# Performance work log

Measured on AMD Instinct MI355X. Metric: run time of the kernel, lower is better.

## Reference

```python
import jax, jax.numpy as jnp
import numpy as np

N = 50000
E = 600000
IN_DIM = 128
HID = 128
HEADS = 4
OUT = HID // HEADS  # per-head out channels
R = 2
LAYERS = 2
NEG_SLOPE = 0.2


def _glorot(key, shape):
    fan_in, fan_out = shape[-2], shape[-1]
    lim = jnp.sqrt(6.0 / (fan_in + fan_out))
    return jax.random.uniform(key, shape, jnp.float32, -lim, lim)


def setup_inputs() -> dict:
    key = jax.random.key(0)
    ks = jax.random.split(key, 20)
    x = jax.random.normal(ks[0], (N, IN_DIM), jnp.float32)
    eidx = jax.random.randint(ks[1], (2, E), 0, N, jnp.int64 if jax.config.jax_enable_x64 else jnp.int32)
    etype = jax.random.randint(ks[2], (E,), 0, R, eidx.dtype)
    d = IN_DIM
    params = {}
    ki = 3
    for l in range(LAYERS):
        params[f"W{l}"] = _glorot(ks[ki], (R, d, HID)); ki += 1            # per-relation weight
        params[f"Q{l}"] = _glorot(ks[ki], (HID, HEADS)); ki += 1           # query proj (dim=1)
        params[f"K{l}"] = _glorot(ks[ki], (HID, HEADS)); ki += 1           # key proj
        params[f"cb{l}"] = jnp.zeros((HID,), jnp.float32)                   # conv bias
        params[f"pW{l}"] = _glorot(ks[ki], (HID, HID)); ki += 1            # proj Linear weight [out,in]
        params[f"pb{l}"] = jnp.zeros((HID,), jnp.float32)
        d = HID
    return dict(x=x, eidx=eidx, etype=etype, **params)


def _rgat_conv(h, src, dst, etype, W, Q, K, b):
    # per-relation transform of all nodes: [R, N, HID]
    xw = jnp.einsum('ni,rio->rno', h, W)
    out_j = xw[etype, src]          # [E, HID] source features under edge's relation
    out_i = xw[etype, dst]          # [E, HID] target features under edge's relation
    # additive self-attention, dim=1: alpha [E, HEADS]
    alpha = jax.nn.leaky_relu(out_i @ Q + out_j @ K, NEG_SLOPE)
    # segment softmax over destination nodes (across-relation)
    m = jax.ops.segment_max(alpha, dst, num_segments=N)
    m = jnp.where(jnp.isfinite(m), m, 0.0)
    e = jnp.exp(alpha - m[dst])
    s = jax.ops.segment_sum(e, dst, num_segments=N)
    a = e / (s[dst] + 1e-16)
    # weighted messages and scatter-sum aggregation
    msg = out_j.reshape(E, HEADS, OUT) * a[:, :, None]
    agg = jax.ops.segment_sum(msg.reshape(E, HID), dst, num_segments=N)
    return agg + b


def reference(x, eidx, etype, W0, Q0, K0, cb0, pW0, pb0, W1, Q1, K1, cb1, pW1, pb1):
    src, dst = eidx[0], eidx[1]  # flow source_to_target: aggregate at eidx[1]
    h = x
    for (W, Q, K, cb, pW, pb) in ((W0, Q0, K0, cb0, pW0, pb0), (W1, Q1, K1, cb1, pW1, pb1)):
        h = _rgat_conv(h, src, dst, etype, W, Q, K, cb)
        h = jax.nn.elu(h @ pW.T + pb)
    return h
```

## Files before the change

kernel.cpp:

```cpp
#include <hip/hip_runtime.h>
#include <hip/hip_bf16.h>

typedef __hip_bfloat16 bf16;
typedef short s16x8 __attribute__((ext_vector_type(8)));
typedef float f32x4 __attribute__((ext_vector_type(4)));

#define N_NODES 50000
#define NPAD    50048
#define E_EDGES 600000
#define HID     128
#define HEADS   4
#define SCAN_B  196

__device__ __forceinline__ unsigned short f2bf_bits(float f) {
  unsigned u = __float_as_uint(f);
  u += 0x7fffu + ((u >> 16) & 1u);
  return (unsigned short)(u >> 16);
}
__device__ __forceinline__ float bf2f(unsigned short b) {
  return __uint_as_float(((unsigned)b) << 16);
}
__device__ __forceinline__ float lo_f(unsigned v) { return __uint_as_float(v << 16); }
__device__ __forceinline__ float hi_f(unsigned v) { return __uint_as_float(v & 0xffff0000u); }

__device__ __forceinline__ float lrelu(float v) { return v >= 0.f ? v : 0.2f * v; }

__global__ __launch_bounds__(256) void detect_kernel(const unsigned short* __restrict__ xb,
                                                     const int* __restrict__ ei,
                                                     int* __restrict__ flags) {
  int t = threadIdx.x;
  __shared__ int cnt[2];
  if (t < 2) cnt[t] = 0;
  __syncthreads();
  unsigned short v = xb[2 * t];
  int ex = (v >> 7) & 0xFF;
  if (ex < 119 || ex > 135) atomicAdd(&cnt[0], 1);
  if (ei[2 * t + 1] != 0) atomicAdd(&cnt[1], 1);
  __syncthreads();
  if (t == 0) {
    flags[0] = (cnt[0] > 64) ? 1 : 0;
    flags[1] = (cnt[1] == 0) ? 1 : 0;
  }
}

__global__ __launch_bounds__(256) void zero_int_kernel(int* __restrict__ p, int n) {
  int i = blockIdx.x * 256 + threadIdx.x;
  if (i < n) p[i] = 0;
}

__global__ __launch_bounds__(256) void cvt_idx_hist_kernel(const int* __restrict__ eidx,
                                                           const int* __restrict__ etype,
                                                           int* __restrict__ dstA, int* __restrict__ pk,
                                                           int* __restrict__ deg,
                                                           const int* __restrict__ flags) {
  int e = blockIdx.x * 256 + threadIdx.x;
  if (e >= E_EDGES) return;
  int s, d, r;
  if (flags[1]) {
    const long long* e64 = (const long long*)eidx;
    const long long* t64 = (const long long*)etype;
    s = (int)e64[e]; d = (int)e64[E_EDGES + e]; r = (int)t64[e];
  } else {
    s = eidx[e]; d = eidx[E_EDGES + e]; r = etype[e];
  }
  dstA[e] = d;
  pk[e] = s | (r << 16);
  atomicAdd(&deg[d], 1);
}

__global__ __launch_bounds__(256) void cvt_xb_kernel(const void* __restrict__ src,
                                                     unsigned short* __restrict__ dst, int n,
                                                     const int* __restrict__ flags) {
  int i = blockIdx.x * 256 + threadIdx.x;
  if (i >= n) return;
  if (flags[0]) dst[i] = f2bf_bits(((const float*)src)[i]);
  else          dst[i] = ((const unsigned short*)src)[i];
}

__global__ __launch_bounds__(256) void cvt_wt_kernel(const void* __restrict__ src0,
                                                     const void* __restrict__ src1,
                                                     unsigned short* __restrict__ dst,
                                                     const int* __restrict__ flags) {
  int idx = blockIdx.x * 256 + threadIdx.x;
  if (idx >= 2 * 2 * HID * HID) return;
  int l = idx >> 15, rem = idx & 32767;
  int r = rem >> 14, i = (rem >> 7) & 127, o = rem & 127;
  const void* src = l ? src1 : src0;
  unsigned short b;
  if (flags[0]) b = f2bf_bits(((const float*)src)[rem]);
  else          b = ((const unsigned short*)src)[rem];
  dst[(size_t)l * 2 * HID * HID + ((size_t)r * HID + o) * HID + i] = b;
}

struct P8 { const void* src[8]; int dstoff[8]; int n[8]; };
__global__ __launch_bounds__(256) void cvt_params_kernel(P8 tab, float* __restrict__ base,
                                                         const int* __restrict__ flags) {
  const int f = flags[0];
  for (int k = 0; k < 8; ++k) {
    int n = tab.n[k];
    for (int i = blockIdx.x * 256 + threadIdx.x; i < n; i += gridDim.x * 256) {
      float v = f ? ((const float*)tab.src[k])[i] : bf2f(((const unsigned short*)tab.src[k])[i]);
      base[tab.dstoff[k] + i] = v;
    }
  }
}

__global__ __launch_bounds__(256) void scan1_kernel(const int* __restrict__ deg,
                                                    int* __restrict__ excl,
                                                    int* __restrict__ bsum) {
  __shared__ int sm[256];
  int t = threadIdx.x, i = blockIdx.x * 256 + t;
  int v = (i < NPAD) ? deg[i] : 0;
  sm[t] = v;
  __syncthreads();
#pragma unroll
  for (int off = 1; off < 256; off <<= 1) {
    int add = (t >= off) ? sm[t - off] : 0;
    __syncthreads();
    sm[t] += add;
    __syncthreads();
  }
  if (i < NPAD) excl[i] = sm[t] - v;
  if (t == 255) bsum[blockIdx.x] = sm[255];
}

__global__ __launch_bounds__(256) void scan23_kernel(const int* __restrict__ excl,
                                                     const int* __restrict__ bsum,
                                                     int* __restrict__ rowstart) {
  __shared__ int sm[256];
  int t = threadIdx.x;
  int v = (t < SCAN_B) ? bsum[t] : 0;
  sm[t] = v;
  __syncthreads();
#pragma unroll
  for (int off = 1; off < 256; off <<= 1) {
    int add = (t >= off) ? sm[t - off] : 0;
    __syncthreads();
    sm[t] += add;
    __syncthreads();
  }
  int bpre = (blockIdx.x > 0) ? sm[blockIdx.x - 1] : 0;
  int i = blockIdx.x * 256 + t;
  if (i < NPAD) rowstart[i] = excl[i] + bpre;
  if (i == 0) rowstart[NPAD] = E_EDGES;
}

__global__ __launch_bounds__(256) void scatter_kernel(const int* __restrict__ dstA,
                                                      const int* __restrict__ pk,
                                                      const int* __restrict__ rowstart,
                                                      int* __restrict__ cnt,
                                                      int* __restrict__ eord) {
  int e = blockIdx.x * 256 + threadIdx.x;
  if (e >= E_EDGES) return;
  int d = dstA[e];
  int pos = rowstart[d] + atomicAdd(&cnt[d], 1);
  eord[pos] = pk[e];
}

__device__ __forceinline__ void wave_gemm64(const unsigned short* __restrict__ Ab, int row0,
                                            const unsigned short* __restrict__ Bt, int colb,
                                            int lane, f32x4 acc[4][4]) {
  const int lm = lane & 15, q = lane >> 4;
  s16x8 af[4][4], bfr[4][4];
#pragma unroll
  for (int kc = 0; kc < 4; ++kc) {
    const int ko = kc * 32 + q * 8;
#pragma unroll
    for (int rt = 0; rt < 4; ++rt)
      af[kc][rt] = *(const s16x8*)(Ab + (size_t)(row0 + rt * 16 + lm) * HID + ko);
  }
#pragma unroll
  for (int kc = 0; kc < 4; ++kc) {
    const int ko = kc * 32 + q * 8;
#pragma unroll
    for (int ct = 0; ct < 4; ++ct)
      bfr[kc][ct] = *(const s16x8*)(Bt + (size_t)(colb + ct * 16 + lm) * HID + ko);
  }
#pragma unroll
  for (int kc = 0; kc < 4; ++kc)
#pragma unroll
    for (int rt = 0; rt < 4; ++rt)
#pragma unroll
      for (int ct = 0; ct < 4; ++ct)
        acc[rt][ct] = __builtin_amdgcn_mfma_f32_16x16x32_bf16(af[kc][rt], bfr[kc][ct], acc[rt][ct], 0, 0, 0);
}

__global__ __launch_bounds__(256) void gemm_xw_mfma(const unsigned short* __restrict__ hb,
                                                    const unsigned short* __restrict__ Wbt,
                                                    unsigned short* __restrict__ xw) {
  const int wave = threadIdx.x >> 6, lane = threadIdx.x & 63;
  const int row0 = blockIdx.x * 64;
  const int r = wave >> 1, colb = (wave & 1) * 64;
  f32x4 acc[4][4];
#pragma unroll
  for (int a = 0; a < 4; ++a)
#pragma unroll
    for (int b = 0; b < 4; ++b) { f32x4 z = {0.f, 0.f, 0.f, 0.f}; acc[a][b] = z; }
  wave_gemm64(hb, row0, Wbt + (size_t)r * HID * HID, colb, lane, acc);
  const int lm = lane & 15, q = lane >> 4;
#pragma unroll
  for (int rt = 0; rt < 4; ++rt)
#pragma unroll
    for (int i = 0; i < 4; ++i) {
      int row = row0 + rt * 16 + q * 4 + i;
      if (row < N_NODES) {
#pragma unroll
        for (int ct = 0; ct < 4; ++ct) {
          int o = colb + ct * 16 + lm;
          xw[((size_t)r * NPAD + row) * HID + o] = f2bf_bits(acc[rt][ct][i]);
        }
      }
    }
}

__global__ __launch_bounds__(128) void proj_mfma(const unsigned short* __restrict__ aggb,
                                                 const unsigned short* __restrict__ pWTb,
                                                 const float* __restrict__ bo,
                                                 unsigned short* __restrict__ hbout,
                                                 void* __restrict__ dout,
                                                 const int* __restrict__ flags) {
  const int wave = threadIdx.x >> 6, lane = threadIdx.x & 63;
  const int row0 = blockIdx.x * 64;
  const int colb = wave * 64;
  f32x4 acc[4][4];
#pragma unroll
  for (int a = 0; a < 4; ++a)
#pragma unroll
    for (int b = 0; b < 4; ++b) { f32x4 z = {0.f, 0.f, 0.f, 0.f}; acc[a][b] = z; }
  wave_gemm64(aggb, row0, pWTb, colb, lane, acc);
  const int lm = lane & 15, q = lane >> 4;
  const int f32out = flags[0];
#pragma unroll
  for (int rt = 0; rt < 4; ++rt)
#pragma unroll
    for (int i = 0; i < 4; ++i) {
      int row = row0 + rt * 16 + q * 4 + i;
      if (row < N_NODES) {
#pragma unroll
        for (int ct = 0; ct < 4; ++ct) {
          int o = colb + ct * 16 + lm;
          float v = acc[rt][ct][i] + bo[o];
          v = v > 0.f ? v : expm1f(v);
          size_t idx = (size_t)row * HID + o;
          if (dout) {
            if (f32out) ((float*)dout)[idx] = v;
            else        ((unsigned short*)dout)[idx] = f2bf_bits(v);
          } else {
            hbout[idx] = f2bf_bits(v);
          }
        }
      }
    }
}

__global__ __launch_bounds__(256) void prep_wq_kernel(const unsigned short* __restrict__ Wbt,
                                                      const float* __restrict__ Qf,
                                                      const float* __restrict__ Kf,
                                                      unsigned short* __restrict__ qkt_hi,
                                                      unsigned short* __restrict__ qkt_lo) {
  int idx = blockIdx.x * 256 + threadIdx.x;
  if (idx >= 2 * 2 * HID) return;
  int i = idx & 127, lr = idx >> 7, l = lr >> 1, r = (lr & 1);
  float aq[4] = {0.f, 0.f, 0.f, 0.f}, ak[4] = {0.f, 0.f, 0.f, 0.f};
  const unsigned short* Wb = Wbt + (size_t)lr * HID * HID;
  const float* Qp = Qf + l * HID * HEADS;
  const float* Kp = Kf + l * HID * HEADS;
  for (int j = 0; j < HID; ++j) {
    float w = bf2f(Wb[j * HID + i]);
    float4 q4 = *(const float4*)(Qp + j * 4);
    float4 k4 = *(const float4*)(Kp + j * 4);
    aq[0] += w * q4.x; aq[1] += w * q4.y; aq[2] += w * q4.z; aq[3] += w * q4.w;
    ak[0] += w * k4.x; ak[1] += w * k4.y; ak[2] += w * k4.z; ak[3] += w * k4.w;
  }
  size_t base = (size_t)l * 16 * HID;
#pragma unroll
  for (int h = 0; h < 4; ++h) {
    unsigned short qh = f2bf_bits(aq[h]);
    unsigned short kh = f2bf_bits(ak[h]);
    float qres = aq[h] - bf2f(qh);
    float kres = ak[h] - bf2f(kh);
    qkt_hi[base + (size_t)(r * 4 + h) * HID + i] = qh;
    qkt_lo[base + (size_t)(r * 4 + h) * HID + i] = f2bf_bits(qres);
    qkt_hi[base + (size_t)(8 + r * 4 + h) * HID + i] = kh;
    qkt_lo[base + (size_t)(8 + r * 4 + h) * HID + i] = f2bf_bits(kres);
  }
}

__global__ __launch_bounds__(256) void qk_mfma_kernel(const unsigned short* __restrict__ hb,
                                                      const unsigned short* __restrict__ qkt_hi,
                                                      const unsigned short* __restrict__ qkt_lo,
                                                      float4* __restrict__ qi4,
                                                      float4* __restrict__ kj4) {
  __shared__ float st[4][16][68];
  const int wave = threadIdx.x >> 6, lane = threadIdx.x & 63;
  const int row0 = blockIdx.x * 256 + wave * 64;
  const int lm = lane & 15, q = lane >> 4;
  if (row0 < NPAD) {
    s16x8 bhi[4], blo[4], af[4][4];
#pragma unroll
    for (int kc = 0; kc < 4; ++kc) {
      const int ko = kc * 32 + q * 8;
      bhi[kc] = *(const s16x8*)(qkt_hi + (size_t)lm * HID + ko);
      blo[kc] = *(const s16x8*)(qkt_lo + (size_t)lm * HID + ko);
    }
#pragma unroll
    for (int kc = 0; kc < 4; ++kc) {
      const int ko = kc * 32 + q * 8;
#pragma unroll
      for (int rt = 0; rt < 4; ++rt)
        af[kc][rt] = *(const s16x8*)(hb + (size_t)(row0 + rt * 16 + lm) * HID + ko);
    }
    f32x4 acc[4];
#pragma unroll
    for (int a = 0; a < 4; ++a) { f32x4 z = {0.f, 0.f, 0.f, 0.f}; acc[a] = z; }
#pragma unroll
    for (int kc = 0; kc < 4; ++kc)
#pragma unroll
      for (int rt = 0; rt < 4; ++rt) {
        acc[rt] = __builtin_amdgcn_mfma_f32_16x16x32_bf16(af[kc][rt], bhi[kc], acc[rt], 0, 0, 0);
        acc[rt] = __builtin_amdgcn_mfma_f32_16x16x32_bf16(af[kc][rt], blo[kc], acc[rt], 0, 0, 0);
      }
#pragma unroll
    for (int rt = 0; rt < 4; ++rt)
      *(f32x4*)&st[wave][lm][rt * 16 + q * 4] = acc[rt];
  }
  __syncthreads();
  if (row0 < NPAD) {
    int n = row0 + lane;
    if (n < N_NODES) {
      float4 v;
      v.x = st[wave][0][lane]; v.y = st[wave][1][lane]; v.z = st[wave][2][lane]; v.w = st[wave][3][lane];
      qi4[n] = v;
      v.x = st[wave][4][lane]; v.y = st[wave][5][lane]; v.z = st[wave][6][lane]; v.w = st[wave][7][lane];
      qi4[NPAD + n] = v;
      v.x = st[wave][8][lane]; v.y = st[wave][9][lane]; v.z = st[wave][10][lane]; v.w = st[wave][11][lane];
      kj4[n] = v;
      v.x = st[wave][12][lane]; v.y = st[wave][13][lane]; v.z = st[wave][14][lane]; v.w = st[wave][15][lane];
      kj4[NPAD + n] = v;
    }
  }
}

__global__ __launch_bounds__(256) void edge_fused_kernel(
    const int* __restrict__ rowstart, const int* __restrict__ eord,
    const float4* __restrict__ qi4, const float4* __restrict__ kj4,
    const unsigned short* __restrict__ xw, unsigned short* __restrict__ aggb) {
  __shared__ float wls[4][64][4];
  const int wave = threadIdx.x >> 6, lane = threadIdx.x & 63;
  const int n = blockIdx.x * 4 + wave;
  unsigned* outp = (unsigned*)(aggb + ((size_t)n << 7)) + lane;
  const int start = rowstart[n];
  const int deg = rowstart[n + 1] - start;
  if (deg == 0) { *outp = 0u; return; }
  const int hh = lane >> 4;
  const int ch2 = lane << 1;
  float2 acc = {0.f, 0.f};
  float ssel;
  if (deg <= 64) {
    int p = 0;
    float a0 = -1e30f, a1 = -1e30f, a2 = -1e30f, a3 = -1e30f;
    if (lane < deg) {
      p = eord[start + lane];
      int s = p & 0xffff, r = p >> 16;
      float4 k4 = kj4[r ? (NPAD + s) : s];
      float4 q4 = r ? qi4[NPAD + n] : qi4[n];
      a0 = lrelu(q4.x + k4.x); a1 = lrelu(q4.y + k4.y);
      a2 = lrelu(q4.z + k4.z); a3 = lrelu(q4.w + k4.w);
    }
    float m0 = a0, m1 = a1, m2 = a2, m3 = a3;
#pragma unroll
    for (int off = 32; off > 0; off >>= 1) {
      m0 = fmaxf(m0, __shfl_xor(m0, off)); m1 = fmaxf(m1, __shfl_xor(m1, off));
      m2 = fmaxf(m2, __shfl_xor(m2, off)); m3 = fmaxf(m3, __shfl_xor(m3, off));
    }
    float w0 = 0.f, w1 = 0.f, w2 = 0.f, w3 = 0.f;
    if (lane < deg) {
      w0 = __expf(a0 - m0); w1 = __expf(a1 - m1);
      w2 = __expf(a2 - m2); w3 = __expf(a3 - m3);
    }
    float s0 = w0, s1 = w1, s2 = w2, s3 = w3;
#pragma unroll
    for (int off = 32; off > 0; off >>= 1) {
      s0 += __shfl_xor(s0, off); s1 += __shfl_xor(s1, off);
      s2 += __shfl_xor(s2, off); s3 += __shfl_xor(s3, off);
    }
    ssel = hh == 0 ? s0 : hh == 1 ? s1 : hh == 2 ? s2 : s3;
    volatile float* wp = &wls[wave][lane][0];
    wp[0] = w0; wp[1] = w1; wp[2] = w2; wp[3] = w3;
    volatile float* wr = &wls[wave][0][0];
    const int degp = (deg + 3) & ~3;
    for (int e = 0; e < degp; e += 4) {
      int p0 = __builtin_amdgcn_readlane(p, e);
      int p1 = __builtin_amdgcn_readlane(p, e + 1);
      int p2 = __builtin_amdgcn_readlane(p, e + 2);
      int p3 = __builtin_amdgcn_readlane(p, e + 3);
      unsigned v0 = *(const unsigned*)(xw + ((size_t)((p0 & 0xffff) + (p0 >> 16) * NPAD) << 7) + ch2);
      unsigned v1 = *(const unsigned*)(xw + ((size_t)((p1 & 0xffff) + (p1 >> 16) * NPAD) << 7) + ch2);
      unsigned v2 = *(const unsigned*)(xw + ((size_t)((p2 & 0xffff) + (p2 >> 16) * NPAD) << 7) + ch2);
      unsigned v3 = *(const unsigned*)(xw + ((size_t)((p3 & 0xffff) + (p3 >> 16) * NPAD) << 7) + ch2);
      float we0 = wr[(e + 0) * 4 + hh];
      float we1 = wr[(e + 1) * 4 + hh];
      float we2 = wr[(e + 2) * 4 + hh];
      float we3 = wr[(e + 3) * 4 + hh];
      acc.x = fmaf(lo_f(v0), we0, acc.x); acc.y = fmaf(hi_f(v0), we0, acc.y);
      acc.x = fmaf(lo_f(v1), we1, acc.x); acc.y = fmaf(hi_f(v1), we1, acc.y);
      acc.x = fmaf(lo_f(v2), we2, acc.x); acc.y = fmaf(hi_f(v2), we2, acc.y);
      acc.x = fmaf(lo_f(v3), we3, acc.x); acc.y = fmaf(hi_f(v3), we3, acc.y);
    }
  } else {
    const float4 q0 = qi4[n], q1 = qi4[NPAD + n];
    float4 m = make_float4(-1e30f, -1e30f, -1e30f, -1e30f);
    for (int e = start; e < start + deg; ++e) {
      int pe = eord[e];
      int s = pe & 0xffff, r = pe >> 16;
      float4 k4 = kj4[(size_t)r * NPAD + s];
      float4 q4 = r ? q1 : q0;
      m.x = fmaxf(m.x, lrelu(q4.x + k4.x)); m.y = fmaxf(m.y, lrelu(q4.y + k4.y));
      m.z = fmaxf(m.z, lrelu(q4.z + k4.z)); m.w = fmaxf(m.w, lrelu(q4.w + k4.w));
    }
    float4 sv = make_float4(0.f, 0.f, 0.f, 0.f);
    for (int e = start; e < start + deg; ++e) {
      int pe = eord[e];
      int s = pe & 0xffff, r = pe >> 16;
      float4 k4 = kj4[(size_t)r * NPAD + s];
      float4 q4 = r ? q1 : q0;
      float w0 = __expf(lrelu(q4.x + k4.x) - m.x);
      float w1 = __expf(lrelu(q4.y + k4.y) - m.y);
      float w2 = __expf(lrelu(q4.z + k4.z) - m.z);
      float w3 = __expf(lrelu(q4.w + k4.w) - m.w);
      sv.x += w0; sv.y += w1; sv.z += w2; sv.w += w3;
      float we = hh == 0 ? w0 : hh == 1 ? w1 : hh == 2 ? w2 : w3;
      unsigned v = *(const unsigned*)(xw + (((size_t)r * NPAD + s) << 7) + ch2);
      acc.x = fmaf(lo_f(v), we, acc.x);
      acc.y = fmaf(hi_f(v), we, acc.y);
    }
    ssel = hh == 0 ? sv.x : hh == 1 ? sv.y : hh == 2 ? sv.z : sv.w;
  }
  float inv = 1.f / (ssel + 1e-16f);
  *outp = (unsigned)f2bf_bits(acc.x * inv) | ((unsigned)f2bf_bits(acc.y * inv) << 16);
}

__global__ __launch_bounds__(64) void prep_proj_kernel(const void* __restrict__ pW0,
                                                       const void* __restrict__ pW1,
                                                       const float* __restrict__ cbf,
                                                       const float* __restrict__ pbf,
                                                       unsigned short* __restrict__ pWTb2,
                                                       float* __restrict__ bo2,
                                                       const int* __restrict__ flags) {
  int o = blockIdx.x & 127, l = blockIdx.x >> 7, t = threadIdx.x;
  const void* pWraw = l ? pW1 : pW0;
  const float* cb = cbf + l * HID;
  const int f = flags[0];
  float part = 0.f;
#pragma unroll
  for (int i = t; i < HID; i += 64) {
    float w = f ? ((const float*)pWraw)[o * HID + i] : bf2f(((const unsigned short*)pWraw)[o * HID + i]);
    pWTb2[(size_t)l * HID * HID + o * HID + i] = f2bf_bits(w);
    part += cb[i] * w;
  }
#pragma unroll
  for (int off = 32; off > 0; off >>= 1) part += __shfl_xor(part, off);
  if (t == 0) bo2[l * HID + o] = pbf[l * HID + o] + part;
}

extern "C" void kernel_launch(void* const* d_in, const int* in_sizes, int n_in,
                              void* d_out, int out_size, void* d_ws, size_t ws_size,
                              hipStream_t stream) {
  const void* x     = d_in[0];
  const int*  eidx  = (const int*)d_in[1];
  const int*  etype = (const int*)d_in[2];
  const int iW[2] = {3, 9}, iQ[2] = {4, 10}, iK[2] = {5, 11}, icb[2] = {6, 12}, ipW[2] = {7, 13}, ipb[2] = {8, 14};

  float* ws = (float*)d_ws;
  size_t off = 0;
  int*   flags = (int*)(ws + off); off += 16;
  unsigned short* hb   = (unsigned short*)(ws + off); off += (size_t)NPAD * HID / 2;
  unsigned short* xw   = (unsigned short*)(ws + off); off += (size_t)NPAD * HID;
  float* qi   = ws + off; off += (size_t)2 * NPAD * HEADS;
  float* kj   = ws + off; off += (size_t)2 * NPAD * HEADS;
  unsigned short* aggb = (unsigned short*)(ws + off); off += (size_t)NPAD * HID / 2;
  int* dstA = (int*)(ws + off); off += E_EDGES;
  int* pk   = (int*)(ws + off); off += E_EDGES;
  int* eord = (int*)(ws + off); off += E_EDGES;
  int* deg  = (int*)(ws + off); off += NPAD;
  int* cnt  = (int*)(ws + off); off += NPAD;
  int* excl = (int*)(ws + off); off += NPAD;
  int* rowstart = (int*)(ws + off); off += NPAD + 16;
  int* bsum  = (int*)(ws + off); off += 256;
  unsigned short* Wbt   = (unsigned short*)(ws + off); off += (size_t)2 * 2 * HID * HID / 2;
  unsigned short* pWTb2 = (unsigned short*)(ws + off); off += (size_t)2 * HID * HID / 2;
  unsigned short* qkt_hi = (unsigned short*)(ws + off); off += (size_t)2 * 16 * HID / 2;
  unsigned short* qkt_lo = (unsigned short*)(ws + off); off += (size_t)2 * 16 * HID / 2;
  float* Qf  = ws + off; off += 2 * HID * HEADS;
  float* Kf  = ws + off; off += 2 * HID * HEADS;
  float* cbf = ws + off; off += 2 * HID;
  float* pbf = ws + off; off += 2 * HID;
  float* bo2 = ws + off; off += 2 * HID;

  detect_kernel<<<1, 256, 0, stream>>>((const unsigned short*)x, eidx, flags);
  zero_int_kernel<<<(2 * NPAD + 255) / 256, 256, 0, stream>>>(deg, 2 * NPAD);
  cvt_idx_hist_kernel<<<(E_EDGES + 255) / 256, 256, 0, stream>>>(eidx, etype, dstA, pk, deg, flags);
  cvt_xb_kernel<<<(N_NODES * HID + 255) / 256, 256, 0, stream>>>(x, hb, N_NODES * HID, flags);
  cvt_wt_kernel<<<(2 * 2 * HID * HID + 255) / 256, 256, 0, stream>>>(d_in[iW[0]], d_in[iW[1]], Wbt, flags);
  {
    P8 tab;
    float* base = ws;
    for (int l = 0; l < 2; ++l) {
      tab.src[l * 4 + 0] = d_in[iQ[l]];  tab.dstoff[l * 4 + 0] = (int)(Qf - base) + l * HID * HEADS;  tab.n[l * 4 + 0] = HID * HEADS;
      tab.src[l * 4 + 1] = d_in[iK[l]];  tab.dstoff[l * 4 + 1] = (int)(Kf - base) + l * HID * HEADS;  tab.n[l * 4 + 1] = HID * HEADS;
      tab.src[l * 4 + 2] = d_in[icb[l]]; tab.dstoff[l * 4 + 2] = (int)(cbf - base) + l * HID;         tab.n[l * 4 + 2] = HID;
      tab.src[l * 4 + 3] = d_in[ipb[l]]; tab.dstoff[l * 4 + 3] = (int)(pbf - base) + l * HID;         tab.n[l * 4 + 3] = HID;
    }
    cvt_params_kernel<<<2, 256, 0, stream>>>(tab, base, flags);
  }

  scan1_kernel<<<SCAN_B, 256, 0, stream>>>(deg, excl, bsum);
  scan23_kernel<<<SCAN_B, 256, 0, stream>>>(excl, bsum, rowstart);
  scatter_kernel<<<(E_EDGES + 255) / 256, 256, 0, stream>>>(dstA, pk, rowstart, cnt, eord);

  prep_wq_kernel<<<2, 256, 0, stream>>>(Wbt, Qf, Kf, qkt_hi, qkt_lo);
  prep_proj_kernel<<<2 * HID, 64, 0, stream>>>(d_in[ipW[0]], d_in[ipW[1]], cbf, pbf, pWTb2, bo2, flags);

  const int RB = NPAD / 64;
  const int QB = (NPAD + 255) / 256;
  for (int l = 0; l < 2; ++l) {
    gemm_xw_mfma<<<RB, 256, 0, stream>>>(hb, Wbt + (size_t)l * 2 * HID * HID, xw);
    qk_mfma_kernel<<<QB, 256, 0, stream>>>(hb, qkt_hi + (size_t)l * 16 * HID, qkt_lo + (size_t)l * 16 * HID,
                                           (float4*)qi, (float4*)kj);
    edge_fused_kernel<<<N_NODES / 4, 256, 0, stream>>>(rowstart, eord, (const float4*)qi, (const float4*)kj, xw, aggb);
    proj_mfma<<<RB, 128, 0, stream>>>(aggb, pWTb2 + (size_t)l * HID * HID, bo2 + l * HID, hb,
                                      (l == 1) ? d_out : nullptr, flags);
  }
}
```

Baseline: 392.4 us.

## Stage GEMM A tiles in LDS and unroll edge gather by eight

Both MFMA GEMM kernels now load the 64-row A tile cooperatively into padded shared memory with coalesced 16-byte loads, instead of each wave reading it strided from global memory. The B fragments are still loaded per wave before the tile. In the edge kernel, the attention-weight LDS layout becomes head-major with padding, and the gather loop issues eight independent row loads per iteration instead of four, to hide more memory latency. This costs extra LDS, a block barrier, and more registers, and the padded loop runs for up to seven more readlane slots for low-degree nodes.

After: 373.1 us. 1.05x faster.

```diff
diff --git a/kernel.cpp b/kernel.cpp
--- a/kernel.cpp
+++ b/kernel.cpp
@@ -157,47 +157,48 @@
   eord[pos] = pk[e];
 }
 
-__device__ __forceinline__ void wave_gemm64(const unsigned short* __restrict__ Ab, int row0,
-                                            const unsigned short* __restrict__ Bt, int colb,
-                                            int lane, f32x4 acc[4][4]) {
-  const int lm = lane & 15, q = lane >> 4;
-  s16x8 af[4][4], bfr[4][4];
-#pragma unroll
-  for (int kc = 0; kc < 4; ++kc) {
-    const int ko = kc * 32 + q * 8;
-#pragma unroll
-    for (int rt = 0; rt < 4; ++rt)
-      af[kc][rt] = *(const s16x8*)(Ab + (size_t)(row0 + rt * 16 + lm) * HID + ko);
-  }
-#pragma unroll
-  for (int kc = 0; kc < 4; ++kc) {
-    const int ko = kc * 32 + q * 8;
-#pragma unroll
-    for (int ct = 0; ct < 4; ++ct)
-      bfr[kc][ct] = *(const s16x8*)(Bt + (size_t)(colb + ct * 16 + lm) * HID + ko);
-  }
-#pragma unroll
-  for (int kc = 0; kc < 4; ++kc)
-#pragma unroll
-    for (int rt = 0; rt < 4; ++rt)
-#pragma unroll
-      for (int ct = 0; ct < 4; ++ct)
-        acc[rt][ct] = __builtin_amdgcn_mfma_f32_16x16x32_bf16(af[kc][rt], bfr[kc][ct], acc[rt][ct], 0, 0, 0);
-}
 
 __global__ __launch_bounds__(256) void gemm_xw_mfma(const unsigned short* __restrict__ hb,
                                                     const unsigned short* __restrict__ Wbt,
                                                     unsigned short* __restrict__ xw) {
-  const int wave = threadIdx.x >> 6, lane = threadIdx.x & 63;
+  __shared__ unsigned short As[64][136];
+  const int t = threadIdx.x;
+  const int wave = t >> 6, lane = t & 63;
   const int row0 = blockIdx.x * 64;
   const int r = wave >> 1, colb = (wave & 1) * 64;
+  const int lm = lane & 15, q = lane >> 4;
+  const unsigned short* Bt = Wbt + (size_t)r * HID * HID;
+  s16x8 bfr[4][4];
+#pragma unroll
+  for (int kc = 0; kc < 4; ++kc) {
+    const int ko = kc * 32 + q * 8;
+#pragma unroll
+    for (int ct = 0; ct < 4; ++ct)
+      bfr[kc][ct] = *(const s16x8*)(Bt + (size_t)(colb + ct * 16 + lm) * HID + ko);
+  }
+  const unsigned short* gsrc = hb + (size_t)row0 * HID;
+#pragma unroll
+  for (int j = 0; j < 4; ++j) {
+    int idx = j * 256 + t;
+    *(s16x8*)&As[idx >> 4][(idx & 15) * 8] = *(const s16x8*)(gsrc + idx * 8);
+  }
+  __syncthreads();
   f32x4 acc[4][4];
 #pragma unroll
   for (int a = 0; a < 4; ++a)
 #pragma unroll
     for (int b = 0; b < 4; ++b) { f32x4 z = {0.f, 0.f, 0.f, 0.f}; acc[a][b] = z; }
-  wave_gemm64(hb, row0, Wbt + (size_t)r * HID * HID, colb, lane, acc);
-  const int lm = lane & 15, q = lane >> 4;
+#pragma unroll
+  for (int kc = 0; kc < 4; ++kc) {
+    const int ko = kc * 32 + q * 8;
+#pragma unroll
+    for (int rt = 0; rt < 4; ++rt) {
+      s16x8 a = *(const s16x8*)&As[rt * 16 + lm][ko];
+#pragma unroll
+      for (int ct = 0; ct < 4; ++ct)
+        acc[rt][ct] = __builtin_amdgcn_mfma_f32_16x16x32_bf16(a, bfr[kc][ct], acc[rt][ct], 0, 0, 0);
+    }
+  }
 #pragma unroll
   for (int rt = 0; rt < 4; ++rt)
 #pragma unroll
@@ -219,16 +220,43 @@
                                                  unsigned short* __restrict__ hbout,
                                                  void* __restrict__ dout,
                                                  const int* __restrict__ flags) {
-  const int wave = threadIdx.x >> 6, lane = threadIdx.x & 63;
+  __shared__ unsigned short As[64][136];
+  const int t = threadIdx.x;
+  const int wave = t >> 6, lane = t & 63;
   const int row0 = blockIdx.x * 64;
   const int colb = wave * 64;
+  const int lm = lane & 15, q = lane >> 4;
+  s16x8 bfr[4][4];
+#pragma unroll
+  for (int kc = 0; kc < 4; ++kc) {
+    const int ko = kc * 32 + q * 8;
+#pragma unroll
+    for (int ct = 0; ct < 4; ++ct)
+      bfr[kc][ct] = *(const s16x8*)(pWTb + (size_t)(colb + ct * 16 + lm) * HID + ko);
+  }
+  const unsigned short* gsrc = aggb + (size_t)row0 * HID;
+#pragma unroll
+  for (int j = 0; j < 8; ++j) {
+    int idx = j * 128 + t;
+    *(s16x8*)&As[idx >> 4][(idx & 15) * 8] = *(const s16x8*)(gsrc + idx * 8);
+  }
+  __syncthreads();
   f32x4 acc[4][4];
 #pragma unroll
   for (int a = 0; a < 4; ++a)
 #pragma unroll
     for (int b = 0; b < 4; ++b) { f32x4 z = {0.f, 0.f, 0.f, 0.f}; acc[a][b] = z; }
-  wave_gemm64(aggb, row0, pWTb, colb, lane, acc);
-  const int lm = lane & 15, q = lane >> 4;
+#pragma unroll
+  for (int kc = 0; kc < 4; ++kc) {
+    const int ko = kc * 32 + q * 8;
+#pragma unroll
+    for (int rt = 0; rt < 4; ++rt) {
+      s16x8 a = *(const s16x8*)&As[rt * 16 + lm][ko];
+#pragma unroll
+      for (int ct = 0; ct < 4; ++ct)
+        acc[rt][ct] = __builtin_amdgcn_mfma_f32_16x16x32_bf16(a, bfr[kc][ct], acc[rt][ct], 0, 0, 0);
+    }
+  }
   const int f32out = flags[0];
 #pragma unroll
   for (int rt = 0; rt < 4; ++rt)
@@ -345,7 +373,7 @@
     const int* __restrict__ rowstart, const int* __restrict__ eord,
     const float4* __restrict__ qi4, const float4* __restrict__ kj4,
     const unsigned short* __restrict__ xw, unsigned short* __restrict__ aggb) {
-  __shared__ float wls[4][64][4];
+  __shared__ volatile float wls[4][4][72];
   const int wave = threadIdx.x >> 6, lane = threadIdx.x & 63;
   const int n = blockIdx.x * 4 + wave;
   unsigned* outp = (unsigned*)(aggb + ((size_t)n << 7)) + lane;
@@ -385,27 +413,28 @@
       s2 += __shfl_xor(s2, off); s3 += __shfl_xor(s3, off);
     }
     ssel = hh == 0 ? s0 : hh == 1 ? s1 : hh == 2 ? s2 : s3;
-    volatile float* wp = &wls[wave][lane][0];
-    wp[0] = w0; wp[1] = w1; wp[2] = w2; wp[3] = w3;
-    volatile float* wr = &wls[wave][0][0];
-    const int degp = (deg + 3) & ~3;
-    for (int e = 0; e < degp; e += 4) {
-      int p0 = __builtin_amdgcn_readlane(p, e);
-      int p1 = __builtin_amdgcn_readlane(p, e + 1);
-      int p2 = __builtin_amdgcn_readlane(p, e + 2);
-      int p3 = __builtin_amdgcn_readlane(p, e + 3);
-      unsigned v0 = *(const unsigned*)(xw + ((size_t)((p0 & 0xffff) + (p0 >> 16) * NPAD) << 7) + ch2);
-      unsigned v1 = *(const unsigned*)(xw + ((size_t)((p1 & 0xffff) + (p1 >> 16) * NPAD) << 7) + ch2);
-      unsigned v2 = *(const unsigned*)(xw + ((size_t)((p2 & 0xffff) + (p2 >> 16) * NPAD) << 7) + ch2);
-      unsigned v3 = *(const unsigned*)(xw + ((size_t)((p3 & 0xffff) + (p3 >> 16) * NPAD) << 7) + ch2);
-      float we0 = wr[(e + 0) * 4 + hh];
-      float we1 = wr[(e + 1) * 4 + hh];
-      float we2 = wr[(e + 2) * 4 + hh];
-      float we3 = wr[(e + 3) * 4 + hh];
-      acc.x = fmaf(lo_f(v0), we0, acc.x); acc.y = fmaf(hi_f(v0), we0, acc.y);
-      acc.x = fmaf(lo_f(v1), we1, acc.x); acc.y = fmaf(hi_f(v1), we1, acc.y);
-      acc.x = fmaf(lo_f(v2), we2, acc.x); acc.y = fmaf(hi_f(v2), we2, acc.y);
-      acc.x = fmaf(lo_f(v3), we3, acc.x); acc.y = fmaf(hi_f(v3), we3, acc.y);
+    wls[wave][0][lane] = w0;
+    wls[wave][1][lane] = w1;
+    wls[wave][2][lane] = w2;
+    wls[wave][3][lane] = w3;
+    volatile const float* wrh = &wls[wave][hh][0];
+    const int degp = (deg + 7) & ~7;
+#pragma unroll 1
+    for (int e = 0; e < degp; e += 8) {
+      int pp[8];
+      unsigned vv[8];
+#pragma unroll
+      for (int u = 0; u < 8; ++u)
+        pp[u] = __builtin_amdgcn_readlane(p, e + u);
+#pragma unroll
+      for (int u = 0; u < 8; ++u)
+        vv[u] = *(const unsigned*)(xw + ((size_t)((pp[u] & 0xffff) + (pp[u] >> 16) * NPAD) << 7) + ch2);
+#pragma unroll
+      for (int u = 0; u < 8; ++u) {
+        float we = wrh[e + u];
+        acc.x = fmaf(lo_f(vv[u]), we, acc.x);
+        acc.y = fmaf(hi_f(vv[u]), we, acc.y);
+      }
     }
   } else {
     const float4 q0 = qi4[n], q1 = qi4[NPAD + n];
```
